# Optimization experiments

Measured on AMD Instinct MI355X. Metric: run time of the kernel, lower is better.

## Reference

```python
import jax, jax.numpy as jnp
import numpy as np

DEPTH, DIM, HEADS, DH, MLP, N, B = 6, 192, 12, 16, 768, 256, 32
INNER = HEADS * DH  # 192


def setup_inputs() -> dict:
    key = jax.random.key(0)
    ks = jax.random.split(key, 10)
    w = lambda i, shape: jax.random.normal(ks[i], shape, dtype=jnp.float32) * 0.02
    return {
        'x': jax.random.normal(ks[0], (B, N, DIM), dtype=jnp.float32),
        'ln1_g': jnp.ones((DEPTH, DIM), jnp.float32),
        'ln1_b': jnp.zeros((DEPTH, DIM), jnp.float32),
        'Wq': w(1, (DEPTH, DIM, INNER)),
        'Wkv': w(2, (DEPTH, DIM, 2 * INNER)),
        'lsa_scale': jnp.full((DEPTH, HEADS), DH ** -0.5, dtype=jnp.float32),
        'mix_pre': jax.random.normal(ks[3], (DEPTH, HEADS, HEADS), dtype=jnp.float32),
        'mix_post': jax.random.normal(ks[4], (DEPTH, HEADS, HEADS), dtype=jnp.float32),
        'Wo': w(5, (DEPTH, INNER, DIM)),
        'bo': jnp.zeros((DEPTH, DIM), jnp.float32),
        'ls1': jnp.full((DEPTH, DIM), 0.1, dtype=jnp.float32),
        'ln2_g': jnp.ones((DEPTH, DIM), jnp.float32),
        'ln2_b': jnp.zeros((DEPTH, DIM), jnp.float32),
        'W1': w(6, (DEPTH, DIM, MLP)),
        'b1': jnp.zeros((DEPTH, MLP), jnp.float32),
        'W2': w(7, (DEPTH, MLP, DIM)),
        'b2': jnp.zeros((DEPTH, DIM), jnp.float32),
        'ls2': jnp.full((DEPTH, DIM), 0.1, dtype=jnp.float32),
    }


def _ln(x, g, b, eps=1e-5):
    m = x.mean(-1, keepdims=True)
    v = ((x - m) ** 2).mean(-1, keepdims=True)
    return (x - m) * jax.lax.rsqrt(v + eps) * g + b


def _heads(t, b, n):
    # (b, n, h*d) -> (b, h, n, d)
    return t.reshape(b, n, HEADS, DH).transpose(0, 2, 1, 3)


def _forward(x, ln1_g, ln1_b, Wq, Wkv, lsa_scale, mix_pre, mix_post, Wo, bo,
             ls1, ln2_g, ln2_b, W1, b1, W2, b2, ls2):
    b, n, _ = x.shape
    diag = jnp.arange(n)
    for l in range(DEPTH):
        # --- PreNorm + talking-heads LSA attention + LayerScale(0.1) ---
        h = _ln(x, ln1_g[l], ln1_b[l])
        q = _heads(h @ Wq[l], b, n)
        k, v = jnp.split(h @ Wkv[l], 2, axis=-1)
        k, v = _heads(k, b, n), _heads(v, b, n)
        dots = jnp.einsum('bhid,bhjd->bhij', q, k) * lsa_scale[l][None, :, None, None]
        # LSA: source sets diagonal to -1e-09 (literal, near-zero) when if_patch_attn
        dots = dots.at[:, :, diag, diag].set(-1e-9)
        dots = jnp.einsum('bhij,hg->bgij', dots, mix_pre[l])
        a = jax.nn.softmax(dots, axis=-1)
        a = jnp.einsum('bhij,hg->bgij', a, mix_post[l])
        o = jnp.einsum('bhij,bhjd->bhid', a, v)
        o = o.transpose(0, 2, 1, 3).reshape(b, n, INNER) @ Wo[l] + bo[l]
        x = x + o * ls1[l]
        # --- PreNorm + GELU FFN + LayerScale(0.1) ---
        h2 = _ln(x, ln2_g[l], ln2_b[l])
        f = jax.nn.gelu(h2 @ W1[l] + b1[l], approximate=False) @ W2[l] + b2[l]
        x = x + f * ls2[l]
    return x


def reference(x, ln1_g, ln1_b, Wq, Wkv, lsa_scale, mix_pre, mix_post, Wo, bo,
              ls1, ln2_g, ln2_b, W1, b1, W2, b2, ls2):
    return _forward(x, ln1_g, ln1_b, Wq, Wkv, lsa_scale, mix_pre, mix_post, Wo,
                    bo, ls1, ln2_g, ln2_b, W1, b1, W2, b2, ls2)
```

## Files before the change

kernel.cpp:

```cpp
#include <hip/hip_runtime.h>
#include <hip/hip_bf16.h>

#define DEPTH   6
#define DIM     192
#define HEADS   12
#define DH      16
#define MLPD    768
#define SEQ     256
#define BATCH   32
#define ROWS    (BATCH*SEQ)

typedef __attribute__((ext_vector_type(8))) short short8;
typedef __attribute__((ext_vector_type(4))) float f32x4;
typedef __attribute__((ext_vector_type(4))) _Float16 half4;
typedef __attribute__((ext_vector_type(8))) _Float16 half8;
typedef __hip_bfloat16 bf16_t;
typedef _Float16 f16_t;

__device__ __forceinline__ bf16_t f2b(float v){ return __float2bfloat16(v); }
__device__ __forceinline__ ushort f2u(float v){
    union{ bf16_t b; ushort u; } w; w.b = __float2bfloat16(v); return w.u;
}
__device__ __forceinline__ f16_t u2h(ushort u){ union{ ushort u; f16_t h; } w; w.u = u; return w.h; }
__device__ __forceinline__ ushort h2u(f16_t h){ union{ ushort u; f16_t h; } w; w.h = h; return w.u; }

__device__ __forceinline__ void async16(ushort* lds, const ushort* gp){
    __builtin_amdgcn_global_load_lds(
        (const __attribute__((address_space(1))) uint*)gp,
        (__attribute__((address_space(3))) uint*)lds, 16, 0, 0);
}

__global__ void copy_kernel(const float* __restrict__ x, float* __restrict__ xr, int n){
    int i = blockIdx.x*256 + threadIdx.x;
    if (i < n) xr[i] = x[i];
}

__device__ __forceinline__ void wt_tile(const float* __restrict__ W,
        ushort* __restrict__ WT, int K, int N, int l, int tx, int ty,
        int tid, ushort* T){
    const float* src = W + ((size_t)l*K + tx*64)*N + ty*64;
    ushort* dst = WT + ((size_t)l*N + ty*64)*K + tx*64;
    int r = tid >> 2, c4 = (tid & 3)*16;
    #pragma unroll
    for (int u=0; u<4; u++){
        float4 v = *(const float4*)(src + (size_t)r*N + c4 + u*4);
        T[(c4+u*4+0)*72 + r] = f2u(v.x);
        T[(c4+u*4+1)*72 + r] = f2u(v.y);
        T[(c4+u*4+2)*72 + r] = f2u(v.z);
        T[(c4+u*4+3)*72 + r] = f2u(v.w);
    }
    __syncthreads();
    int n = tid >> 2, k8 = (tid & 3)*16;
    #pragma unroll
    for (int u=0; u<2; u++)
        *(uint4*)(dst + (size_t)n*K + k8 + u*8) = *(uint4*)&T[n*72 + k8 + u*8];
}

__global__ __launch_bounds__(256) void wt_all(
        const float* __restrict__ Wq, const float* __restrict__ Wkv,
        const float* __restrict__ Wo, const float* __restrict__ W1,
        const float* __restrict__ W2,
        ushort* __restrict__ WqT, ushort* __restrict__ WkvT,
        ushort* __restrict__ WoT, ushort* __restrict__ W1T,
        ushort* __restrict__ W2T){
    __shared__ ushort T[64*72];
    int id = blockIdx.x, l = blockIdx.y, tid = threadIdx.x;
    if (id < 9)       wt_tile(Wq,  WqT,  192, 192, l, id/3,       id%3,       tid, T);
    else if (id < 27) wt_tile(Wkv, WkvT, 192, 384, l, (id-9)/6,   (id-9)%6,   tid, T);
    else if (id < 36) wt_tile(Wo,  WoT,  192, 192, l, (id-27)/3,  (id-27)%3,  tid, T);
    else if (id < 72) wt_tile(W1,  W1T,  192, 768, l, (id-36)/12, (id-36)%12, tid, T);
    else              wt_tile(W2,  W2T,  768, 192, l, (id-72)/3,  (id-72)%3,  tid, T);
}

__global__ __launch_bounds__(256) void ln_kernel(
        const float* __restrict__ xres, const float* __restrict__ ln_g,
        const float* __restrict__ ln_b, ushort* __restrict__ out){
    int lane = threadIdx.x & 63, w = threadIdx.x >> 6;
    int row = blockIdx.x*4 + w;
    const float* xr = xres + (size_t)row*DIM;
    float v0 = xr[lane], v1 = xr[lane+64], v2 = xr[lane+128];
    float s = v0+v1+v2;
    #pragma unroll
    for (int off=32; off; off>>=1) s += __shfl_xor(s, off, 64);
    float m = s*(1.0f/192.0f);
    float d0=v0-m, d1=v1-m, d2=v2-m;
    float q = d0*d0+d1*d1+d2*d2;
    #pragma unroll
    for (int off=32; off; off>>=1) q += __shfl_xor(q, off, 64);
    float inv = rsqrtf(q*(1.0f/192.0f) + 1e-5f);
    float g0 = ln_g[lane], g1 = ln_g[lane+64], g2 = ln_g[lane+128];
    float e0 = ln_b[lane], e1 = ln_b[lane+64], e2 = ln_b[lane+128];
    ushort* dst = out + (size_t)row*DIM;
    dst[lane]     = f2u(d0*inv*g0 + e0);
    dst[lane+64]  = f2u(d1*inv*g1 + e1);
    dst[lane+128] = f2u(d2*inv*g2 + e2);
}

template<int MODE>
__global__ __launch_bounds__(256) void gemm_ln_kernel(
        const ushort* __restrict__ Aln, const ushort* __restrict__ BT0,
        const ushort* __restrict__ BT1, const float* __restrict__ bias,
        f16_t* __restrict__ out0, f16_t* __restrict__ out1,
        f16_t* __restrict__ out2){
    __shared__ ushort As[6*2048];
    __shared__ ushort Bs[6*2048];
    int tid = threadIdx.x, lane = tid & 63, w = tid >> 6;
    int bm = blockIdx.x*64;
    int bn = blockIdx.y*64;
    {
        const ushort* ap = Aln + (size_t)(bm + (tid>>2))*DIM + (tid&3)*8;
        const ushort* bt; int bnl;
        if (MODE == 0 && bn >= DIM){ bt = BT1; bnl = bn - DIM; }
        else { bt = BT0; bnl = bn; }
        const ushort* bp = bt + (size_t)(bnl + (tid>>2))*DIM + (tid&3)*8;
        #pragma unroll
        for (int c=0; c<6; c++){
            async16(&As[c*2048 + tid*8], ap + c*32);
            async16(&Bs[c*2048 + tid*8], bp + c*32);
        }
    }
    __syncthreads();
    int wrow = w >> 1, wcol = w & 1;
    int quad = lane >> 4, mr = lane & 15;
    f32x4 acc[2][2] = {};
    #pragma unroll
    for (int c = 0; c < 6; c++){
        short8 a0 = *(const short8*)&As[c*2048 + (wrow*32+mr)*32    + quad*8];
        short8 a1 = *(const short8*)&As[c*2048 + (wrow*32+16+mr)*32 + quad*8];
        short8 b0 = *(const short8*)&Bs[c*2048 + (wcol*32+mr)*32    + quad*8];
        short8 b1 = *(const short8*)&Bs[c*2048 + (wcol*32+16+mr)*32 + quad*8];
        acc[0][0] = __builtin_amdgcn_mfma_f32_16x16x32_bf16(a0, b0, acc[0][0], 0,0,0);
        acc[0][1] = __builtin_amdgcn_mfma_f32_16x16x32_bf16(a0, b1, acc[0][1], 0,0,0);
        acc[1][0] = __builtin_amdgcn_mfma_f32_16x16x32_bf16(a1, b0, acc[1][0], 0,0,0);
        acc[1][1] = __builtin_amdgcn_mfma_f32_16x16x32_bf16(a1, b1, acc[1][1], 0,0,0);
    }
    #pragma unroll
    for (int rr=0; rr<2; rr++){
        #pragma unroll
        for (int cc=0; cc<2; cc++){
            int col = bn + wcol*32 + cc*16 + mr;
            if (MODE == 0){
                if (col < 2*DIM){
                    f16_t* op = (col < DIM) ? (out0 + col) : (out1 + col - DIM);
                    #pragma unroll
                    for (int tt=0; tt<4; tt++){
                        int row = bm + wrow*32 + rr*16 + quad*4 + tt;
                        op[(size_t)row*DIM] = (f16_t)acc[rr][cc][tt];
                    }
                } else {
                    int d = col - 2*DIM;
                    int row0 = bm + wrow*32 + rr*16 + quad*4;
                    int bb = row0 >> 8, j0 = row0 & 255;
                    half4 pk;
                    #pragma unroll
                    for (int tt=0; tt<4; tt++) pk[tt] = (f16_t)acc[rr][cc][tt];
                    *(half4*)(out2 + (((size_t)(bb*DIM + d)) << 8) + j0) = pk;
                }
            } else {
                float bv = bias[col];
                #pragma unroll
                for (int tt=0; tt<4; tt++){
                    int row = bm + wrow*32 + rr*16 + quad*4 + tt;
                    float z = acc[rr][cc][tt] + bv;
                    ((bf16_t*)out0)[(size_t)row*MLPD + col] =
                        f2b(0.5f*z*(1.0f + erff(z*0.70710678118654752f)));
                }
            }
        }
    }
}

template<int ROUNDS>
__global__ __launch_bounds__(256) void gemm_a_kernel(
        const ushort* __restrict__ A, const ushort* __restrict__ BT,
        const float* __restrict__ bias, const float* __restrict__ ls,
        float* __restrict__ xres){
    const int K = ROUNDS*192;
    __shared__ ushort As[6*2048];
    __shared__ ushort Bs[6*2048];
    int tid = threadIdx.x, lane = tid & 63, w = tid >> 6;
    int wrow = w >> 1, wcol = w & 1;
    int bm = blockIdx.x*64, bn = blockIdx.y*64;
    int quad = lane >> 4, mr = lane & 15;
    const ushort* ap = A  + (size_t)(bm + (tid>>2))*K + (tid&3)*8;
    const ushort* bp = BT + (size_t)(bn + (tid>>2))*K + (tid&3)*8;
    f32x4 acc[2][2] = {};
    for (int r = 0; r < ROUNDS; r++){
        #pragma unroll
        for (int c=0; c<6; c++){
            async16(&As[c*2048 + tid*8], ap + r*192 + c*32);
            async16(&Bs[c*2048 + tid*8], bp + r*192 + c*32);
        }
        __syncthreads();
        #pragma unroll
        for (int c=0; c<6; c++){
            short8 a0 = *(const short8*)&As[c*2048 + (wrow*32+mr)*32    + quad*8];
            short8 a1 = *(const short8*)&As[c*2048 + (wrow*32+16+mr)*32 + quad*8];
            short8 b0 = *(const short8*)&Bs[c*2048 + (wcol*32+mr)*32    + quad*8];
            short8 b1 = *(const short8*)&Bs[c*2048 + (wcol*32+16+mr)*32 + quad*8];
            acc[0][0] = __builtin_amdgcn_mfma_f32_16x16x32_bf16(a0, b0, acc[0][0], 0,0,0);
            acc[0][1] = __builtin_amdgcn_mfma_f32_16x16x32_bf16(a0, b1, acc[0][1], 0,0,0);
            acc[1][0] = __builtin_amdgcn_mfma_f32_16x16x32_bf16(a1, b0, acc[1][0], 0,0,0);
            acc[1][1] = __builtin_amdgcn_mfma_f32_16x16x32_bf16(a1, b1, acc[1][1], 0,0,0);
        }
        if (r+1 < ROUNDS) __syncthreads();
    }
    #pragma unroll
    for (int rr=0; rr<2; rr++){
        #pragma unroll
        for (int cc=0; cc<2; cc++){
            int col = bn + wcol*32 + cc*16 + mr;
            float bv = bias[col], lv = ls[col];
            #pragma unroll
            for (int tt=0; tt<4; tt++){
                int row = bm + wrow*32 + rr*16 + quad*4 + tt;
                xres[(size_t)row*DIM + col] += (acc[rr][cc][tt] + bv)*lv;
            }
        }
    }
}

#define SLAB    4488
#define IST     280
#define KV_OFF  53856
#define VJP     72
#define ROWP    200
#define Q_OFF   67680
#define POST_OFF 70880
#define PRE_OFF 71136
#define LTOT    71808

__global__ __launch_bounds__(1024, 1) void attn_kernel(
        const f16_t* __restrict__ qb, const f16_t* __restrict__ kb,
        const f16_t* __restrict__ vTg,
        const float* __restrict__ lsa, const float* __restrict__ pre,
        const float* __restrict__ post, const ushort* __restrict__ WoT,
        const float* __restrict__ bo, const float* __restrict__ ls1,
        float* __restrict__ xres){
    __shared__ ushort L[LTOT];
    int tid  = threadIdx.x;
    int lane = tid & 63, w = tid >> 6;
    int quad = lane >> 4, nr = lane & 15;
    int b  = blockIdx.x >> 4;
    int i0 = (blockIdx.x & 15) << 4;

    {
        uint* Z = (uint*)&L[KV_OFF];
        for (int k = tid; k < (LTOT - KV_OFF)/2; k += 1024) Z[k] = 0;
    }
    __syncthreads();

    if (tid < 384){
        int e = tid*8, i = e/DIM, d = e%DIM, hh = d >> 4;
        float sc = lsa[hh];
        union { uint4 v; f16_t h[8]; } iv, ov;
        iv.v = *(const uint4*)(qb + (size_t)(b*SEQ + i0 + i)*DIM + d);
        #pragma unroll
        for (int u=0; u<8; u++) ov.h[u] = (f16_t)((float)iv.h[u]*sc);
        *(uint4*)&L[Q_OFF + i*ROWP + d] = ov.v;
    } else if (tid < 512){
        for (int k = tid-384; k < 256; k += 128){
            int gg = k >> 4, hh = k & 15;
            if (gg < 12 && hh < 12)
                L[POST_OFF + k] = h2u((f16_t)post[hh*12+gg]);
        }
    } else if (tid < 640){
        for (int k = tid-512; k < 144; k += 128)
            L[PRE_OFF + k] = h2u((f16_t)pre[k]);
    }
    auto stage_v = [&](int c){
        for (int u = tid; u < 1536; u += 1024){
            int e = u*8;
            int d = e >> 6, j = e & 63;
            uint4 v = *(const uint4*)(vTg + (((size_t)(b*DIM + d)) << 8) + c*64 + j);
            *(uint4*)&L[KV_OFF + d*VJP + j] = v;
        }
    };
    __syncthreads();

    half4 postTf = *(const half4*)&L[POST_OFF + nr*16 + quad*4];

    {
        int jg = w*16 + nr;
        const f16_t* krow = kb + (size_t)(b*SEQ + jg)*DIM;
        half8 qh[6], kh[6];
        #pragma unroll
        for (int c=0; c<6; c++){
            union{ short8 s; half8 h; } a, k2;
            a.s  = *(const short8*)&L[Q_OFF + nr*ROWP + c*32 + quad*8];
            k2.s = *(const short8*)(const void*)(krow + c*32 + quad*8);
            qh[c] = a.h; kh[c] = k2.h;
        }
        int dd = jg - (i0 + quad*4);
        int hb = (quad>>1)*12;
        #pragma unroll
        for (int g=0; g<12; g++){
            f32x4 a = {0,0,0,0};
            #pragma unroll
            for (int c=0; c<6; c++){
                f16_t s = u2h(L[PRE_OFF + hb + c*24 + g]);
                a = __builtin_amdgcn_mfma_f32_16x16x32_f16(qh[c]*s, kh[c], a, 0,0,0);
            }
            ushort* sp = &L[g*SLAB + jg];
            sp[(quad*4+0)*IST] = (dd==0) ? (ushort)0 : h2u((f16_t)a[0]);
            sp[(quad*4+1)*IST] = (dd==1) ? (ushort)0 : h2u((f16_t)a[1]);
            sp[(quad*4+2)*IST] = (dd==2) ? (ushort)0 : h2u((f16_t)a[2]);
            sp[(quad*4+3)*IST] = (dd==3) ? (ushort)0 : h2u((f16_t)a[3]);
        }
    }
    __syncthreads();

    for (int r = w; r < 192; r += 16){
        int g = r >> 4, i = r & 15;
        ushort* sp = &L[g*SLAB + i*IST];
        ushort4 uv = *(ushort4*)&sp[lane*4];
        float e0 = __expf((float)u2h(uv.x));
        float e1 = __expf((float)u2h(uv.y));
        float e2 = __expf((float)u2h(uv.z));
        float e3 = __expf((float)u2h(uv.w));
        float ssum = e0+e1+e2+e3;
        #pragma unroll
        for (int off=32; off; off>>=1) ssum += __shfl_xor(ssum, off, 64);
        float rin = 1.0f/ssum;
        uv.x = h2u((f16_t)(e0*rin)); uv.y = h2u((f16_t)(e1*rin));
        uv.z = h2u((f16_t)(e2*rin)); uv.w = h2u((f16_t)(e3*rin));
        *(ushort4*)&sp[lane*4] = uv;
    }
    __syncthreads();

    for (int s = 0; s < 16; s++){
        int cb = s*16 + w;
        int i = cb >> 4, jb = cb & 15;
        int colbase = i*IST + jb*16 + nr;
        half4 bv;
        #pragma unroll
        for (int t=0; t<4; t++) bv[t] = u2h(L[(quad*4+t)*SLAB + colbase]);
        f32x4 cc = __builtin_amdgcn_mfma_f32_16x16x16f16(postTf, bv, (f32x4){0,0,0,0}, 0,0,0);
        if (quad < 3){
            #pragma unroll
            for (int t=0; t<4; t++) L[(quad*4+t)*SLAB + colbase] = h2u((f16_t)cc[t]);
        }
    }
    __syncthreads();

    f32x4 oacc = {0,0,0,0};
    for (int c = 0; c < 4; c++){
        stage_v(c);
        __syncthreads();
        if (w < 12){
            int g = w;
            #pragma unroll
            for (int ks = 0; ks < 4; ks++){
                int jl = ks*16 + quad*4;
                half4 av = *(const half4*)&L[g*SLAB + nr*IST + c*64 + jl];
                half4 bv = *(const half4*)&L[KV_OFF + (g*16 + nr)*VJP + jl];
                oacc = __builtin_amdgcn_mfma_f32_16x16x16f16(av, bv, oacc, 0,0,0);
            }
        }
        __syncthreads();
    }

    if (w < 12){
        int g = w;
        #pragma unroll
        for (int t=0; t<4; t++){
            int i = quad*4 + t;
            L[Q_OFF + i*ROWP + g*16 + nr] = f2u(oacc[t]);
        }
    }
    __syncthreads();

    if (w < 12){
        f32x4 wacc = {0,0,0,0};
        int ct = w;
        const ushort* wg = WoT + (size_t)(ct*16 + nr)*192;
        #pragma unroll
        for (int c = 0; c < 3; c++){
            #pragma unroll
            for (int sub = 0; sub < 2; sub++){
                int k0 = c*64 + sub*32;
                short8 av = *(const short8*)&L[Q_OFF + nr*ROWP + k0 + quad*8];
                short8 bv = *(const short8*)(wg + k0 + quad*8);
                wacc = __builtin_amdgcn_mfma_f32_16x16x32_bf16(av, bv, wacc, 0,0,0);
            }
        }
        int col = ct*16 + nr;
        float bv2 = bo[col], lv = ls1[col];
        #pragma unroll
        for (int t=0; t<4; t++){
            int row = b*SEQ + i0 + quad*4 + t;
            xres[(size_t)row*DIM + col] += (wacc[t] + bv2)*lv;
        }
    }
}

extern "C" void kernel_launch(void* const* d_in, const int* in_sizes, int n_in,
                              void* d_out, int out_size, void* d_ws, size_t ws_size,
                              hipStream_t stream){
    const float* x    = (const float*)d_in[0];
    const float* ln1g = (const float*)d_in[1];
    const float* ln1b = (const float*)d_in[2];
    const float* Wq   = (const float*)d_in[3];
    const float* Wkv  = (const float*)d_in[4];
    const float* lsa  = (const float*)d_in[5];
    const float* pre  = (const float*)d_in[6];
    const float* post = (const float*)d_in[7];
    const float* Wo   = (const float*)d_in[8];
    const float* bo   = (const float*)d_in[9];
    const float* ls1  = (const float*)d_in[10];
    const float* ln2g = (const float*)d_in[11];
    const float* ln2b = (const float*)d_in[12];
    const float* W1   = (const float*)d_in[13];
    const float* b1   = (const float*)d_in[14];
    const float* W2   = (const float*)d_in[15];
    const float* b2   = (const float*)d_in[16];
    const float* ls2  = (const float*)d_in[17];
    float* xres = (float*)d_out;

    char* ws = (char*)d_ws;
    f16_t*  qb  = (f16_t*)ws;
    f16_t*  kb  = (f16_t*)(ws + (size_t)ROWS*DIM*2);
    f16_t*  vT  = (f16_t*)(ws + (size_t)ROWS*DIM*4);
    bf16_t* fb  = (bf16_t*)ws;
    char* p = ws + (size_t)ROWS*MLPD*2;
    ushort* WqT  = (ushort*)p; p += (size_t)DEPTH*DIM*DIM*2;
    ushort* WkvT = (ushort*)p; p += (size_t)DEPTH*DIM*2*DIM*2;
    ushort* WoT  = (ushort*)p; p += (size_t)DEPTH*DIM*DIM*2;
    ushort* W1T  = (ushort*)p; p += (size_t)DEPTH*DIM*MLPD*2;
    ushort* W2T  = (ushort*)p; p += (size_t)DEPTH*MLPD*DIM*2;
    ushort* lnb  = (ushort*)p; p += (size_t)ROWS*DIM*2;

    int ntot = ROWS*DIM;
    copy_kernel<<<ntot/256, 256, 0, stream>>>(x, xres, ntot);
    wt_all<<<dim3(108, 6), 256, 0, stream>>>(Wq, Wkv, Wo, W1, W2,
                                             WqT, WkvT, WoT, W1T, W2T);
    for (int l = 0; l < DEPTH; l++){
        ln_kernel<<<ROWS/4, 256, 0, stream>>>(xres, ln1g + l*DIM, ln1b + l*DIM, lnb);
        gemm_ln_kernel<0><<<dim3(128,9), 256, 0, stream>>>(lnb,
                WqT + (size_t)l*DIM*DIM, WkvT + (size_t)l*DIM*2*DIM,
                nullptr, qb, kb, vT);
        attn_kernel<<<BATCH*(SEQ/16), 1024, 0, stream>>>(qb, kb, vT,
                lsa + l*HEADS, pre + l*HEADS*HEADS, post + l*HEADS*HEADS,
                WoT + (size_t)l*DIM*DIM, bo + l*DIM, ls1 + l*DIM, xres);
        ln_kernel<<<ROWS/4, 256, 0, stream>>>(xres, ln2g + l*DIM, ln2b + l*DIM, lnb);
        gemm_ln_kernel<1><<<dim3(128,12), 256, 0, stream>>>(lnb,
                W1T + (size_t)l*DIM*MLPD, nullptr, b1 + l*MLPD, (f16_t*)fb, nullptr,
                nullptr);
        gemm_a_kernel<4><<<dim3(128,3), 256, 0, stream>>>((const ushort*)fb,
                W2T + (size_t)l*MLPD*DIM, b2 + l*DIM, ls2 + l*DIM, xres);
    }
}
```

Before: 615.2 us.

## Fuse LN2 into attention epilogue and read V directly from global memory

The attention kernel now computes the post-attention LayerNorm in its epilogue. It stages the updated residual rows in shared memory and writes the bf16 normalized rows, which removes the separate ln_kernel launch and its re-read of xres. V is read straight from global memory per wave instead of being staged through shared memory in four chunks. That drops the zero-fill and several block-wide barriers and shrinks the LDS footprint, in exchange for uncoalesced-ish global V loads in the PV MFMA loop. The post-mix padding is handled by clamping head indices and zeroing explicitly instead of zero-filling LDS.

```diff
diff --git a/kernel.cpp b/kernel.cpp
--- a/kernel.cpp
+++ b/kernel.cpp
@@ -220,15 +220,14 @@
     }
 }
 
-#define SLAB    4488
-#define IST     280
-#define KV_OFF  53856
-#define VJP     72
-#define ROWP    200
-#define Q_OFF   67680
-#define POST_OFF 70880
-#define PRE_OFF 71136
-#define LTOT    71808
+#define SLAB     4488
+#define IST      280
+#define ROWP     200
+#define Q_OFF    53856
+#define POST_OFF 57056
+#define PRE_OFF  57312
+#define X_OFF    57456
+#define LTOT     63856
 
 __global__ __launch_bounds__(1024, 1) void attn_kernel(
         const f16_t* __restrict__ qb, const f16_t* __restrict__ kb,
@@ -236,7 +235,8 @@
         const float* __restrict__ lsa, const float* __restrict__ pre,
         const float* __restrict__ post, const ushort* __restrict__ WoT,
         const float* __restrict__ bo, const float* __restrict__ ls1,
-        float* __restrict__ xres){
+        const float* __restrict__ ln2g, const float* __restrict__ ln2b,
+        ushort* __restrict__ lnb, float* __restrict__ xres){
     __shared__ ushort L[LTOT];
     int tid  = threadIdx.x;
     int lane = tid & 63, w = tid >> 6;
@@ -244,12 +244,6 @@
     int b  = blockIdx.x >> 4;
     int i0 = (blockIdx.x & 15) << 4;
 
-    {
-        uint* Z = (uint*)&L[KV_OFF];
-        for (int k = tid; k < (LTOT - KV_OFF)/2; k += 1024) Z[k] = 0;
-    }
-    __syncthreads();
-
     if (tid < 384){
         int e = tid*8, i = e/DIM, d = e%DIM, hh = d >> 4;
         float sc = lsa[hh];
@@ -261,21 +255,13 @@
     } else if (tid < 512){
         for (int k = tid-384; k < 256; k += 128){
             int gg = k >> 4, hh = k & 15;
-            if (gg < 12 && hh < 12)
-                L[POST_OFF + k] = h2u((f16_t)post[hh*12+gg]);
+            L[POST_OFF + k] = (gg < 12 && hh < 12) ? h2u((f16_t)post[hh*12+gg])
+                                                   : (ushort)0;
         }
     } else if (tid < 640){
         for (int k = tid-512; k < 144; k += 128)
             L[PRE_OFF + k] = h2u((f16_t)pre[k]);
     }
-    auto stage_v = [&](int c){
-        for (int u = tid; u < 1536; u += 1024){
-            int e = u*8;
-            int d = e >> 6, j = e & 63;
-            uint4 v = *(const uint4*)(vTg + (((size_t)(b*DIM + d)) << 8) + c*64 + j);
-            *(uint4*)&L[KV_OFF + d*VJP + j] = v;
-        }
-    };
     __syncthreads();
 
     half4 postTf = *(const half4*)&L[POST_OFF + nr*16 + quad*4];
@@ -334,7 +320,10 @@
         int colbase = i*IST + jb*16 + nr;
         half4 bv;
         #pragma unroll
-        for (int t=0; t<4; t++) bv[t] = u2h(L[(quad*4+t)*SLAB + colbase]);
+        for (int t=0; t<4; t++){
+            int hs = quad*4 + t; if (hs > 11) hs = 11;
+            bv[t] = u2h(L[hs*SLAB + colbase]);
+        }
         f32x4 cc = __builtin_amdgcn_mfma_f32_16x16x16f16(postTf, bv, (f32x4){0,0,0,0}, 0,0,0);
         if (quad < 3){
             #pragma unroll
@@ -344,20 +333,19 @@
     __syncthreads();
 
     f32x4 oacc = {0,0,0,0};
-    for (int c = 0; c < 4; c++){
-        stage_v(c);
-        __syncthreads();
-        if (w < 12){
-            int g = w;
+    if (w < 12){
+        int g = w;
+        const f16_t* vrow = vTg + (((size_t)(b*DIM + g*16 + nr)) << 8);
+        #pragma unroll
+        for (int c = 0; c < 4; c++){
             #pragma unroll
             for (int ks = 0; ks < 4; ks++){
-                int jl = ks*16 + quad*4;
-                half4 av = *(const half4*)&L[g*SLAB + nr*IST + c*64 + jl];
-                half4 bv = *(const half4*)&L[KV_OFF + (g*16 + nr)*VJP + jl];
+                int jl = c*64 + ks*16 + quad*4;
+                half4 av = *(const half4*)&L[g*SLAB + nr*IST + jl];
+                half4 bv = *(const half4*)(vrow + jl);
                 oacc = __builtin_amdgcn_mfma_f32_16x16x16f16(av, bv, oacc, 0,0,0);
             }
         }
-        __syncthreads();
     }
 
     if (w < 12){
@@ -370,6 +358,7 @@
     }
     __syncthreads();
 
+    float* X = (float*)&L[X_OFF];
     if (w < 12){
         f32x4 wacc = {0,0,0,0};
         int ct = w;
@@ -388,9 +377,33 @@
         float bv2 = bo[col], lv = ls1[col];
         #pragma unroll
         for (int t=0; t<4; t++){
-            int row = b*SEQ + i0 + quad*4 + t;
-            xres[(size_t)row*DIM + col] += (wacc[t] + bv2)*lv;
-        }
+            int i = quad*4 + t;
+            int row = b*SEQ + i0 + i;
+            float upd = xres[(size_t)row*DIM + col] + (wacc[t] + bv2)*lv;
+            xres[(size_t)row*DIM + col] = upd;
+            X[i*200 + col] = upd;
+        }
+    }
+    __syncthreads();
+
+    {
+        int i = w;
+        float v0 = X[i*200 + lane], v1 = X[i*200 + lane+64], v2 = X[i*200 + lane+128];
+        float s = v0+v1+v2;
+        #pragma unroll
+        for (int off=32; off; off>>=1) s += __shfl_xor(s, off, 64);
+        float m = s*(1.0f/192.0f);
+        float d0=v0-m, d1=v1-m, d2=v2-m;
+        float q = d0*d0+d1*d1+d2*d2;
+        #pragma unroll
+        for (int off=32; off; off>>=1) q += __shfl_xor(q, off, 64);
+        float inv = rsqrtf(q*(1.0f/192.0f) + 1e-5f);
+        float g0 = ln2g[lane], g1 = ln2g[lane+64], g2 = ln2g[lane+128];
+        float e0 = ln2b[lane], e1 = ln2b[lane+64], e2 = ln2b[lane+128];
+        ushort* dst = lnb + (size_t)(b*SEQ + i0 + i)*DIM;
+        dst[lane]     = f2u(d0*inv*g0 + e0);
+        dst[lane+64]  = f2u(d1*inv*g1 + e1);
+        dst[lane+128] = f2u(d2*inv*g2 + e2);
     }
 }
 
@@ -441,8 +454,8 @@
                 nullptr, qb, kb, vT);
         attn_kernel<<<BATCH*(SEQ/16), 1024, 0, stream>>>(qb, kb, vT,
                 lsa + l*HEADS, pre + l*HEADS*HEADS, post + l*HEADS*HEADS,
-                WoT + (size_t)l*DIM*DIM, bo + l*DIM, ls1 + l*DIM, xres);
-        ln_kernel<<<ROWS/4, 256, 0, stream>>>(xres, ln2g + l*DIM, ln2b + l*DIM, lnb);
+                WoT + (size_t)l*DIM*DIM, bo + l*DIM, ls1 + l*DIM,
+                ln2g + l*DIM, ln2b + l*DIM, lnb, xres);
         gemm_ln_kernel<1><<<dim3(128,12), 256, 0, stream>>>(lnb,
                 W1T + (size_t)l*DIM*MLPD, nullptr, b1 + l*MLPD, (f16_t*)fb, nullptr,
                 nullptr);
```

Result: no change. 620.0 us (+0.8%).
